# Optimization experiments

Hardware: AMD Instinct MI355X
Metric: run time of the kernel (lower is better)

The kernel has to match this reference:

```python
import jax, jax.numpy as jnp
import numpy as np

NQ = 4      # n_qubits
NL = 1      # n_layers
IN_DIM = 512
HIDDEN = 256
B = 131072


def _apply_1q(state, gate, q, batched):
    """Apply a single-qubit gate on qubit q. state: [B, 2**NQ] complex.
    gate: [2,2] (shared) or [B,2,2] (per-sample)."""
    Bsz = state.shape[0]
    left, right = 2 ** q, 2 ** (NQ - q - 1)
    s = state.reshape(Bsz, left, 2, right)
    if batched:
        s = jnp.einsum('bij,bljr->blir', gate, s)
    else:
        s = jnp.einsum('ij,bljr->blir', gate, s)
    return s.reshape(Bsz, -1)


def _cnot_adjacent(state, q):
    """CNOT with control q, target q+1 (adjacent wires only)."""
    Bsz = state.shape[0]
    left, right = 2 ** q, 2 ** (NQ - q - 2)
    s = state.reshape(Bsz, left, 2, 2, right)
    # control=0 branch unchanged; control=1 branch has target flipped
    s = jnp.stack([s[:, :, 0], s[:, :, 1, ::-1]], axis=2)
    return s.reshape(Bsz, -1)


def _rot_gate(phi, theta, omega):
    """PennyLane Rot(phi,theta,omega) = RZ(omega) RY(theta) RZ(phi)."""
    c, s = jnp.cos(theta / 2), jnp.sin(theta / 2)
    ep = jnp.exp(-0.5j * (phi + omega).astype(jnp.complex64))
    em = jnp.exp(-0.5j * (phi - omega).astype(jnp.complex64))
    return jnp.array([[1.0, 0.0], [0.0, 0.0]], jnp.complex64) * (ep * c) + \
           jnp.array([[0.0, -1.0], [0.0, 0.0]], jnp.complex64) * (jnp.conj(em) * s) + \
           jnp.array([[0.0, 0.0], [1.0, 0.0]], jnp.complex64) * (em * s) + \
           jnp.array([[0.0, 0.0], [0.0, 1.0]], jnp.complex64) * (jnp.conj(ep) * c)


def quantum_circuit(angles, weights):
    """Batched statevector simulation. angles: [B, NQ] float, weights: [NL, NQ, 3].
    Returns PauliZ expectations per qubit: [B, NQ] float32."""
    Bsz = angles.shape[0]
    state = jnp.zeros((Bsz, 2 ** NQ), jnp.complex64).at[:, 0].set(1.0)
    # Angle embedding: RY(inputs[i]) on wire i
    for q in range(NQ):
        th = angles[:, q] / 2
        c, sn = jnp.cos(th), jnp.sin(th)
        g = jnp.stack([jnp.stack([c, -sn], -1), jnp.stack([sn, c], -1)], -2).astype(jnp.complex64)  # [B,2,2]
        state = _apply_1q(state, g, q, batched=True)
    # Entangling layers
    for l in range(NL):
        for q in range(NQ):
            g = _rot_gate(weights[l, q, 0], weights[l, q, 1], weights[l, q, 2])
            state = _apply_1q(state, g, q, batched=False)
        for q in range(NQ - 1):
            state = _cnot_adjacent(state, q)
    # <Z_q> = p(q=0) - p(q=1)
    probs = (jnp.abs(state) ** 2).reshape((Bsz,) + (2,) * NQ)
    outs = []
    for q in range(NQ):
        pq = jnp.moveaxis(probs, 1 + q, -1).reshape(Bsz, -1, 2).sum(1)
        outs.append(pq[:, 0] - pq[:, 1])
    return jnp.stack(outs, -1).astype(jnp.float32)


def setup_inputs() -> dict:
    key = jax.random.key(0)
    ks = jax.random.split(key, 10)
    sc1 = 1.0 / np.sqrt(IN_DIM)
    sch = 1.0 / np.sqrt(HIDDEN)
    scq = 1.0 / np.sqrt(NQ)
    return {
        'x': jax.random.normal(ks[0], (B, IN_DIM), jnp.float32),
        'W1': jax.random.uniform(ks[1], (IN_DIM, HIDDEN), jnp.float32, -sc1, sc1),
        'b1': jax.random.uniform(ks[2], (HIDDEN,), jnp.float32, -sc1, sc1),
        'qparams': jax.random.normal(ks[3], (NL, NQ, 3), jnp.float32),
        'Wr': jax.random.uniform(ks[4], (NQ, HIDDEN), jnp.float32, -scq, scq),
        'br': jax.random.uniform(ks[5], (HIDDEN,), jnp.float32, -scq, scq),
        'W2': jax.random.uniform(ks[6], (HIDDEN, HIDDEN), jnp.float32, -sch, sch),
        'b2': jax.random.uniform(ks[7], (HIDDEN,), jnp.float32, -sch, sch),
        'W3': jax.random.uniform(ks[8], (HIDDEN, HIDDEN), jnp.float32, -sch, sch),
        'b3': jax.random.uniform(ks[9], (HIDDEN,), jnp.float32, -sch, sch),
    }


def reference(x, W1, b1, qparams, Wr, br, W2, b2, W3, b3):
    # Linear -> ReLU -> (Dropout: identity in eval)
    h = jax.nn.relu(x @ W1 + b1)                       # [B, HIDDEN]
    # QuantumLinear: circuit uses first NQ features as RY angles, then readout
    q = quantum_circuit(h[:, :NQ], qparams)            # [B, NQ]
    h = jax.nn.relu(q @ Wr + br)                       # [B, HIDDEN]
    # depth-2 = 1 extra hidden block
    h = jax.nn.relu(h @ W2 + b2)
    return h @ W3 + b3                                 # [B, HIDDEN]
```

## Files before the change

kernel.cpp:

```cpp
#include <hip/hip_runtime.h>

typedef float  f32x4  __attribute__((ext_vector_type(4)));
typedef short  short8 __attribute__((ext_vector_type(8)));

#define BM   32
#define LPAD 264

__device__ __forceinline__ unsigned short f2bf(float f){
  union { float f; unsigned int u; } v; v.f = f;
  unsigned int u = v.u;
  return (unsigned short)((u + 0x7FFFu + ((u >> 16) & 1u)) >> 16);
}
__device__ __forceinline__ float bf2f(unsigned short h){
  union { unsigned int u; float f; } v; v.u = ((unsigned int)h) << 16;
  return v.f;
}

__global__ __launch_bounds__(256) void prep_kernel(
    const float* __restrict__ W1, const float* __restrict__ W2,
    const float* __restrict__ W3, float* __restrict__ w1c,
    unsigned short* __restrict__ W2H, unsigned short* __restrict__ W3H)
{
  int t = blockIdx.x * 256 + threadIdx.x;
  if (t < 2048) {
    w1c[t] = W1[(t >> 2) * 256 + (t & 3)];
  } else if (t < 2048 + 65536) {
    int f = t - 2048;
    int j = f & 7, lane = (f >> 3) & 63, ks = (f >> 9) & 7, n16 = f >> 12;
    int k = ks * 32 + (lane >> 4) * 8 + j;
    int n = n16 * 16 + (lane & 15);
    W2H[f] = f2bf(W2[k * 256 + n]);
  } else if (t < 2048 + 2 * 65536) {
    int f = t - 2048 - 65536;
    int j = f & 7, lane = (f >> 3) & 63, ks = (f >> 9) & 7, n16 = f >> 12;
    int k = ks * 32 + (lane >> 4) * 8 + j;
    int n = n16 * 16 + (lane & 15);
    W3H[f] = f2bf(W3[k * 256 + n]);
  }
}

__global__ __launch_bounds__(256) void angle_kernel(
    const float* __restrict__ x, const float* __restrict__ b1,
    const float* __restrict__ qp, const float* __restrict__ w1c,
    float* __restrict__ z)
{
  const int row = blockIdx.x * 256 + threadIdx.x;
  const f32x4* xr = (const f32x4*)(x + (size_t)row * 512);
  const f32x4* w1 = (const f32x4*)w1c;
  f32x4 p = {0.f, 0.f, 0.f, 0.f};
  #pragma unroll 8
  for (int i = 0; i < 128; i++) {
    f32x4 xa = xr[i];
    p += xa[0] * w1[4 * i + 0];
    p += xa[1] * w1[4 * i + 1];
    p += xa[2] * w1[4 * i + 2];
    p += xa[3] * w1[4 * i + 3];
  }
  float a0 = fmaxf(p[0] + b1[0], 0.f);
  float a1 = fmaxf(p[1] + b1[1], 0.f);
  float a2 = fmaxf(p[2] + b1[2], 0.f);
  float a3 = fmaxf(p[3] + b1[3], 0.f);

  float g00r[4], g00i[4], g01r[4], g01i[4], g10r[4], g10i[4], g11r[4], g11i[4];
  #pragma unroll
  for (int q = 0; q < 4; q++) {
    float phi = qp[q * 3 + 0], th = qp[q * 3 + 1], om = qp[q * 3 + 2];
    float c = cosf(0.5f * th), s = sinf(0.5f * th);
    float A1 = 0.5f * (phi + om), A2 = 0.5f * (phi - om);
    float c1 = cosf(A1), s1 = sinf(A1), c2 = cosf(A2), s2 = sinf(A2);
    g00r[q] =  c * c1;  g00i[q] = -c * s1;
    g01r[q] = -s * c2;  g01i[q] = -s * s2;
    g10r[q] =  s * c2;  g10i[q] = -s * s2;
    g11r[q] =  c * c1;  g11i[q] =  c * s1;
  }
  float cr0 = cosf(0.5f * a0), sv0 = sinf(0.5f * a0);
  float cr1 = cosf(0.5f * a1), sv1 = sinf(0.5f * a1);
  float cr2 = cosf(0.5f * a2), sv2 = sinf(0.5f * a2);
  float cr3 = cosf(0.5f * a3), sv3 = sinf(0.5f * a3);
  float sr[16], si[16];
  #pragma unroll
  for (int i = 0; i < 16; i++) {
    float v = ((i & 8) ? sv0 : cr0) * ((i & 4) ? sv1 : cr1) *
              ((i & 2) ? sv2 : cr2) * ((i & 1) ? sv3 : cr3);
    sr[i] = v; si[i] = 0.f;
  }
  #pragma unroll
  for (int q = 0; q < 4; q++) {
    const int st = 8 >> q;
    #pragma unroll
    for (int i = 0; i < 16; i++) {
      if (i & st) continue;
      const int i1 = i + st;
      float xr_ = sr[i], xi_ = si[i], yr_ = sr[i1], yi_ = si[i1];
      sr[i]  = g00r[q] * xr_ - g00i[q] * xi_ + g01r[q] * yr_ - g01i[q] * yi_;
      si[i]  = g00r[q] * xi_ + g00i[q] * xr_ + g01r[q] * yi_ + g01i[q] * yr_;
      sr[i1] = g10r[q] * xr_ - g10i[q] * xi_ + g11r[q] * yr_ - g11i[q] * yi_;
      si[i1] = g10r[q] * xi_ + g10i[q] * xr_ + g11r[q] * yi_ + g11i[q] * yr_;
    }
  }
  #pragma unroll
  for (int q = 0; q < 3; q++) {
    const int cb = 8 >> q, tb = 4 >> q;
    #pragma unroll
    for (int i = 0; i < 16; i++) {
      if ((i & cb) && !(i & tb)) {
        const int j = i | tb;
        float t1 = sr[i]; sr[i] = sr[j]; sr[j] = t1;
        float t2 = si[i]; si[i] = si[j]; si[j] = t2;
      }
    }
  }
  float z0 = 0.f, z1 = 0.f, z2 = 0.f, z3 = 0.f;
  #pragma unroll
  for (int i = 0; i < 16; i++) {
    float pb = sr[i] * sr[i] + si[i] * si[i];
    z0 += (i & 8) ? -pb : pb;
    z1 += (i & 4) ? -pb : pb;
    z2 += (i & 2) ? -pb : pb;
    z3 += (i & 1) ? -pb : pb;
  }
  f32x4 zv = {z0, z1, z2, z3};
  ((f32x4*)z)[row] = zv;
}

__global__ __launch_bounds__(256, 4) void mlp_kernel(
    const float* __restrict__ z,  const float* __restrict__ Wr,
    const float* __restrict__ br, const float* __restrict__ b2,
    const float* __restrict__ b3,
    const unsigned short* __restrict__ W2H,
    const unsigned short* __restrict__ W3H,
    float* __restrict__ out)
{
  __shared__ __align__(16) char smem[512 + 2 * BM * LPAD * 2];
  f32x4* zl = (f32x4*)smem;
  unsigned short* a_hi = (unsigned short*)(smem + 512);
  unsigned short* a_lo = (unsigned short*)(smem + 512 + BM * LPAD * 2);
  float* fstage = (float*)(smem + 512);

  const int tid = threadIdx.x;
  const int w = tid >> 6, lane = tid & 63;
  const int l15 = lane & 15, l4 = lane >> 4;
  const int row0 = blockIdx.x * BM;

  if (tid < BM) zl[tid] = ((const f32x4*)z)[row0 + tid];
  __syncthreads();

  {
    float wr0 = Wr[tid], wr1 = Wr[256 + tid], wr2 = Wr[512 + tid], wr3 = Wr[768 + tid];
    float brv = br[tid];
    #pragma unroll 4
    for (int rr = 0; rr < BM; rr++) {
      f32x4 zz = zl[rr];
      float hv = fmaf(zz[0], wr0, fmaf(zz[1], wr1, fmaf(zz[2], wr2, fmaf(zz[3], wr3, brv))));
      hv = fmaxf(hv, 0.f);
      unsigned short hi = f2bf(hv);
      a_hi[rr * LPAD + tid] = hi;
      a_lo[rr * LPAD + tid] = f2bf(hv - bf2f(hi));
    }
  }
  __syncthreads();

  f32x4 acc[2][4];
  #pragma unroll
  for (int m = 0; m < 2; m++)
    #pragma unroll
    for (int n = 0; n < 4; n++) acc[m][n] = 0.f;
  #pragma unroll
  for (int ks = 0; ks < 8; ks++) {
    short8 ah[2], al[2];
    #pragma unroll
    for (int m = 0; m < 2; m++) {
      ah[m] = *(const short8*)&a_hi[(m * 16 + l15) * LPAD + ks * 32 + l4 * 8];
      al[m] = *(const short8*)&a_lo[(m * 16 + l15) * LPAD + ks * 32 + l4 * 8];
    }
    #pragma unroll
    for (int nf = 0; nf < 4; nf++) {
      short8 bh = *(const short8*)&W2H[(size_t)(((w * 4 + nf) * 8 + ks) * 64 + lane) * 8];
      #pragma unroll
      for (int m = 0; m < 2; m++) {
        acc[m][nf] = __builtin_amdgcn_mfma_f32_16x16x32_bf16(ah[m], bh, acc[m][nf], 0, 0, 0);
        acc[m][nf] = __builtin_amdgcn_mfma_f32_16x16x32_bf16(al[m], bh, acc[m][nf], 0, 0, 0);
      }
    }
  }
  __syncthreads();

  #pragma unroll
  for (int nf = 0; nf < 4; nf++) {
    int col = w * 64 + nf * 16 + l15;
    float b2v = b2[col];
    #pragma unroll
    for (int m = 0; m < 2; m++)
      #pragma unroll
      for (int i = 0; i < 4; i++) {
        float hv = fmaxf(acc[m][nf][i] + b2v, 0.f);
        unsigned short hi = f2bf(hv);
        int idx = (m * 16 + l4 * 4 + i) * LPAD + col;
        a_hi[idx] = hi;
        a_lo[idx] = f2bf(hv - bf2f(hi));
      }
  }
  __syncthreads();

  #pragma unroll
  for (int m = 0; m < 2; m++)
    #pragma unroll
    for (int n = 0; n < 4; n++) acc[m][n] = 0.f;
  #pragma unroll
  for (int ks = 0; ks < 8; ks++) {
    short8 ah[2], al[2];
    #pragma unroll
    for (int m = 0; m < 2; m++) {
      ah[m] = *(const short8*)&a_hi[(m * 16 + l15) * LPAD + ks * 32 + l4 * 8];
      al[m] = *(const short8*)&a_lo[(m * 16 + l15) * LPAD + ks * 32 + l4 * 8];
    }
    #pragma unroll
    for (int nf = 0; nf < 4; nf++) {
      short8 bh = *(const short8*)&W3H[(size_t)(((w * 4 + nf) * 8 + ks) * 64 + lane) * 8];
      #pragma unroll
      for (int m = 0; m < 2; m++) {
        acc[m][nf] = __builtin_amdgcn_mfma_f32_16x16x32_bf16(ah[m], bh, acc[m][nf], 0, 0, 0);
        acc[m][nf] = __builtin_amdgcn_mfma_f32_16x16x32_bf16(al[m], bh, acc[m][nf], 0, 0, 0);
      }
    }
  }
  __syncthreads();

  #pragma unroll
  for (int nf = 0; nf < 4; nf++) {
    int col = w * 64 + nf * 16 + l15;
    float b3v = b3[col];
    #pragma unroll
    for (int m = 0; m < 2; m++)
      #pragma unroll
      for (int i = 0; i < 4; i++)
        fstage[(m * 16 + l4 * 4 + i) * 260 + col] = acc[m][nf][i] + b3v;
  }
  __syncthreads();
  #pragma unroll
  for (int rr = 0; rr < 8; rr++) {
    int row = w * 8 + rr;
    f32x4 v = ((const f32x4*)&fstage[row * 260])[lane];
    ((f32x4*)(out + (size_t)(row0 + row) * 256))[lane] = v;
  }
}

extern "C" void kernel_launch(void* const* d_in, const int* in_sizes, int n_in,
                              void* d_out, int out_size, void* d_ws, size_t ws_size,
                              hipStream_t stream)
{
  const float* x  = (const float*)d_in[0];
  const float* W1 = (const float*)d_in[1];
  const float* b1 = (const float*)d_in[2];
  const float* qp = (const float*)d_in[3];
  const float* Wr = (const float*)d_in[4];
  const float* br = (const float*)d_in[5];
  const float* W2 = (const float*)d_in[6];
  const float* b2 = (const float*)d_in[7];
  const float* W3 = (const float*)d_in[8];
  const float* b3 = (const float*)d_in[9];
  float* out = (float*)d_out;

  char* ws = (char*)d_ws;
  float* w1c          = (float*)ws;
  unsigned short* W2H = (unsigned short*)(ws + 8192);
  unsigned short* W3H = (unsigned short*)(ws + 8192 + 1 * 131072);
  float* z            = (float*)(ws + 8192 + 2 * 131072);

  prep_kernel<<<520, 256, 0, stream>>>(W1, W2, W3, w1c, W2H, W3H);
  angle_kernel<<<512, 256, 0, stream>>>(x, b1, qp, w1c, z);
  mlp_kernel<<<4096, 256, 0, stream>>>(z, Wr, br, b2, b3, W2H, W3H, out);
}
```

Measured before the change: 175.6 us.

## Fuse angle/quantum kernel with MLP kernel into one persistent-per-256-rows kernel

Merges the per-row angle and statevector computation with the MFMA MLP into a single kernel. Each block handles 256 rows, computing the quantum expectations into shared memory and then looping over 8 tiles of 32 rows for the readout and the two bf16 split-precision GEMMs. This removes the intermediate z buffer in global memory and one kernel launch. In exchange, the grid shrinks from 4096 to 512 blocks and each block processes its tiles serially, which reduces parallelism and latency hiding.

```diff
diff --git a/kernel.cpp b/kernel.cpp
--- a/kernel.cpp
+++ b/kernel.cpp
@@ -39,209 +39,206 @@
   }
 }
 
-__global__ __launch_bounds__(256) void angle_kernel(
-    const float* __restrict__ x, const float* __restrict__ b1,
+__global__ __launch_bounds__(256) void fused_kernel(
+    const float* __restrict__ x,  const float* __restrict__ b1,
     const float* __restrict__ qp, const float* __restrict__ w1c,
-    float* __restrict__ z)
-{
-  const int row = blockIdx.x * 256 + threadIdx.x;
-  const f32x4* xr = (const f32x4*)(x + (size_t)row * 512);
-  const f32x4* w1 = (const f32x4*)w1c;
-  f32x4 p = {0.f, 0.f, 0.f, 0.f};
-  #pragma unroll 8
-  for (int i = 0; i < 128; i++) {
-    f32x4 xa = xr[i];
-    p += xa[0] * w1[4 * i + 0];
-    p += xa[1] * w1[4 * i + 1];
-    p += xa[2] * w1[4 * i + 2];
-    p += xa[3] * w1[4 * i + 3];
-  }
-  float a0 = fmaxf(p[0] + b1[0], 0.f);
-  float a1 = fmaxf(p[1] + b1[1], 0.f);
-  float a2 = fmaxf(p[2] + b1[2], 0.f);
-  float a3 = fmaxf(p[3] + b1[3], 0.f);
-
-  float g00r[4], g00i[4], g01r[4], g01i[4], g10r[4], g10i[4], g11r[4], g11i[4];
-  #pragma unroll
-  for (int q = 0; q < 4; q++) {
-    float phi = qp[q * 3 + 0], th = qp[q * 3 + 1], om = qp[q * 3 + 2];
-    float c = cosf(0.5f * th), s = sinf(0.5f * th);
-    float A1 = 0.5f * (phi + om), A2 = 0.5f * (phi - om);
-    float c1 = cosf(A1), s1 = sinf(A1), c2 = cosf(A2), s2 = sinf(A2);
-    g00r[q] =  c * c1;  g00i[q] = -c * s1;
-    g01r[q] = -s * c2;  g01i[q] = -s * s2;
-    g10r[q] =  s * c2;  g10i[q] = -s * s2;
-    g11r[q] =  c * c1;  g11i[q] =  c * s1;
-  }
-  float cr0 = cosf(0.5f * a0), sv0 = sinf(0.5f * a0);
-  float cr1 = cosf(0.5f * a1), sv1 = sinf(0.5f * a1);
-  float cr2 = cosf(0.5f * a2), sv2 = sinf(0.5f * a2);
-  float cr3 = cosf(0.5f * a3), sv3 = sinf(0.5f * a3);
-  float sr[16], si[16];
-  #pragma unroll
-  for (int i = 0; i < 16; i++) {
-    float v = ((i & 8) ? sv0 : cr0) * ((i & 4) ? sv1 : cr1) *
-              ((i & 2) ? sv2 : cr2) * ((i & 1) ? sv3 : cr3);
-    sr[i] = v; si[i] = 0.f;
-  }
-  #pragma unroll
-  for (int q = 0; q < 4; q++) {
-    const int st = 8 >> q;
-    #pragma unroll
-    for (int i = 0; i < 16; i++) {
-      if (i & st) continue;
-      const int i1 = i + st;
-      float xr_ = sr[i], xi_ = si[i], yr_ = sr[i1], yi_ = si[i1];
-      sr[i]  = g00r[q] * xr_ - g00i[q] * xi_ + g01r[q] * yr_ - g01i[q] * yi_;
-      si[i]  = g00r[q] * xi_ + g00i[q] * xr_ + g01r[q] * yi_ + g01i[q] * yr_;
-      sr[i1] = g10r[q] * xr_ - g10i[q] * xi_ + g11r[q] * yr_ - g11i[q] * yi_;
-      si[i1] = g10r[q] * xi_ + g10i[q] * xr_ + g11r[q] * yi_ + g11i[q] * yr_;
-    }
-  }
-  #pragma unroll
-  for (int q = 0; q < 3; q++) {
-    const int cb = 8 >> q, tb = 4 >> q;
-    #pragma unroll
-    for (int i = 0; i < 16; i++) {
-      if ((i & cb) && !(i & tb)) {
-        const int j = i | tb;
-        float t1 = sr[i]; sr[i] = sr[j]; sr[j] = t1;
-        float t2 = si[i]; si[i] = si[j]; si[j] = t2;
-      }
-    }
-  }
-  float z0 = 0.f, z1 = 0.f, z2 = 0.f, z3 = 0.f;
-  #pragma unroll
-  for (int i = 0; i < 16; i++) {
-    float pb = sr[i] * sr[i] + si[i] * si[i];
-    z0 += (i & 8) ? -pb : pb;
-    z1 += (i & 4) ? -pb : pb;
-    z2 += (i & 2) ? -pb : pb;
-    z3 += (i & 1) ? -pb : pb;
-  }
-  f32x4 zv = {z0, z1, z2, z3};
-  ((f32x4*)z)[row] = zv;
-}
-
-__global__ __launch_bounds__(256, 4) void mlp_kernel(
-    const float* __restrict__ z,  const float* __restrict__ Wr,
-    const float* __restrict__ br, const float* __restrict__ b2,
-    const float* __restrict__ b3,
+    const float* __restrict__ Wr, const float* __restrict__ br,
+    const float* __restrict__ b2, const float* __restrict__ b3,
     const unsigned short* __restrict__ W2H,
     const unsigned short* __restrict__ W3H,
     float* __restrict__ out)
 {
-  __shared__ __align__(16) char smem[512 + 2 * BM * LPAD * 2];
+  __shared__ __align__(16) char smem[4096 + 2 * BM * LPAD * 2];
   f32x4* zl = (f32x4*)smem;
-  unsigned short* a_hi = (unsigned short*)(smem + 512);
-  unsigned short* a_lo = (unsigned short*)(smem + 512 + BM * LPAD * 2);
-  float* fstage = (float*)(smem + 512);
+  unsigned short* a_hi = (unsigned short*)(smem + 4096);
+  unsigned short* a_lo = (unsigned short*)(smem + 4096 + BM * LPAD * 2);
+  float* fstage = (float*)(smem + 4096);
 
   const int tid = threadIdx.x;
   const int w = tid >> 6, lane = tid & 63;
   const int l15 = lane & 15, l4 = lane >> 4;
-  const int row0 = blockIdx.x * BM;
-
-  if (tid < BM) zl[tid] = ((const f32x4*)z)[row0 + tid];
+  const int row0 = blockIdx.x * 256;
+
+  {
+    const int row = row0 + tid;
+    const f32x4* xr = (const f32x4*)(x + (size_t)row * 512);
+    const f32x4* w1 = (const f32x4*)w1c;
+    f32x4 p = {0.f, 0.f, 0.f, 0.f};
+    #pragma unroll 8
+    for (int i = 0; i < 128; i++) {
+      f32x4 xa = xr[i];
+      p += xa[0] * w1[4 * i + 0];
+      p += xa[1] * w1[4 * i + 1];
+      p += xa[2] * w1[4 * i + 2];
+      p += xa[3] * w1[4 * i + 3];
+    }
+    float a0 = fmaxf(p[0] + b1[0], 0.f);
+    float a1 = fmaxf(p[1] + b1[1], 0.f);
+    float a2 = fmaxf(p[2] + b1[2], 0.f);
+    float a3 = fmaxf(p[3] + b1[3], 0.f);
+
+    float g00r[4], g00i[4], g01r[4], g01i[4], g10r[4], g10i[4], g11r[4], g11i[4];
+    #pragma unroll
+    for (int q = 0; q < 4; q++) {
+      float phi = qp[q * 3 + 0], th = qp[q * 3 + 1], om = qp[q * 3 + 2];
+      float c = cosf(0.5f * th), s = sinf(0.5f * th);
+      float A1 = 0.5f * (phi + om), A2 = 0.5f * (phi - om);
+      float c1 = cosf(A1), s1 = sinf(A1), c2 = cosf(A2), s2 = sinf(A2);
+      g00r[q] =  c * c1;  g00i[q] = -c * s1;
+      g01r[q] = -s * c2;  g01i[q] = -s * s2;
+      g10r[q] =  s * c2;  g10i[q] = -s * s2;
+      g11r[q] =  c * c1;  g11i[q] =  c * s1;
+    }
+    float cr0 = cosf(0.5f * a0), sv0 = sinf(0.5f * a0);
+    float cr1 = cosf(0.5f * a1), sv1 = sinf(0.5f * a1);
+    float cr2 = cosf(0.5f * a2), sv2 = sinf(0.5f * a2);
+    float cr3 = cosf(0.5f * a3), sv3 = sinf(0.5f * a3);
+    float sr[16], si[16];
+    #pragma unroll
+    for (int i = 0; i < 16; i++) {
+      float v = ((i & 8) ? sv0 : cr0) * ((i & 4) ? sv1 : cr1) *
+                ((i & 2) ? sv2 : cr2) * ((i & 1) ? sv3 : cr3);
+      sr[i] = v; si[i] = 0.f;
+    }
+    #pragma unroll
+    for (int q = 0; q < 4; q++) {
+      const int st = 8 >> q;
+      #pragma unroll
+      for (int i = 0; i < 16; i++) {
+        if (i & st) continue;
+        const int i1 = i + st;
+        float xr_ = sr[i], xi_ = si[i], yr_ = sr[i1], yi_ = si[i1];
+        sr[i]  = g00r[q] * xr_ - g00i[q] * xi_ + g01r[q] * yr_ - g01i[q] * yi_;
+        si[i]  = g00r[q] * xi_ + g00i[q] * xr_ + g01r[q] * yi_ + g01i[q] * yr_;
+        sr[i1] = g10r[q] * xr_ - g10i[q] * xi_ + g11r[q] * yr_ - g11i[q] * yi_;
+        si[i1] = g10r[q] * xi_ + g10i[q] * xr_ + g11r[q] * yi_ + g11i[q] * yr_;
+      }
+    }
+    #pragma unroll
+    for (int q = 0; q < 3; q++) {
+      const int cb = 8 >> q, tb = 4 >> q;
+      #pragma unroll
+      for (int i = 0; i < 16; i++) {
+        if ((i & cb) && !(i & tb)) {
+          const int j = i | tb;
+          float t1 = sr[i]; sr[i] = sr[j]; sr[j] = t1;
+          float t2 = si[i]; si[i] = si[j]; si[j] = t2;
+        }
+      }
+    }
+    float z0 = 0.f, z1 = 0.f, z2 = 0.f, z3 = 0.f;
+    #pragma unroll
+    for (int i = 0; i < 16; i++) {
+      float pb = sr[i] * sr[i] + si[i] * si[i];
+      z0 += (i & 8) ? -pb : pb;
+      z1 += (i & 4) ? -pb : pb;
+      z2 += (i & 2) ? -pb : pb;
+      z3 += (i & 1) ? -pb : pb;
+    }
+    f32x4 zv = {z0, z1, z2, z3};
+    zl[tid] = zv;
+  }
   __syncthreads();
 
-  {
-    float wr0 = Wr[tid], wr1 = Wr[256 + tid], wr2 = Wr[512 + tid], wr3 = Wr[768 + tid];
-    float brv = br[tid];
+  const float wr0 = Wr[tid], wr1 = Wr[256 + tid], wr2 = Wr[512 + tid], wr3 = Wr[768 + tid];
+  const float brv = br[tid];
+
+  for (int mt = 0; mt < 8; mt++) {
     #pragma unroll 4
     for (int rr = 0; rr < BM; rr++) {
-      f32x4 zz = zl[rr];
+      f32x4 zz = zl[mt * 32 + rr];
       float hv = fmaf(zz[0], wr0, fmaf(zz[1], wr1, fmaf(zz[2], wr2, fmaf(zz[3], wr3, brv))));
       hv = fmaxf(hv, 0.f);
       unsigned short hi = f2bf(hv);
       a_hi[rr * LPAD + tid] = hi;
       a_lo[rr * LPAD + tid] = f2bf(hv - bf2f(hi));
     }
-  }
-  __syncthreads();
-
-  f32x4 acc[2][4];
-  #pragma unroll
-  for (int m = 0; m < 2; m++)
-    #pragma unroll
-    for (int n = 0; n < 4; n++) acc[m][n] = 0.f;
-  #pragma unroll
-  for (int ks = 0; ks < 8; ks++) {
-    short8 ah[2], al[2];
-    #pragma unroll
-    for (int m = 0; m < 2; m++) {
-      ah[m] = *(const short8*)&a_hi[(m * 16 + l15) * LPAD + ks * 32 + l4 * 8];
-      al[m] = *(const short8*)&a_lo[(m * 16 + l15) * LPAD + ks * 32 + l4 * 8];
-    }
+    __syncthreads();
+
+    f32x4 acc[2][4];
+    #pragma unroll
+    for (int m = 0; m < 2; m++)
+      #pragma unroll
+      for (int n = 0; n < 4; n++) acc[m][n] = 0.f;
+    #pragma unroll
+    for (int ks = 0; ks < 8; ks++) {
+      short8 ah[2], al[2];
+      #pragma unroll
+      for (int m = 0; m < 2; m++) {
+        ah[m] = *(const short8*)&a_hi[(m * 16 + l15) * LPAD + ks * 32 + l4 * 8];
+        al[m] = *(const short8*)&a_lo[(m * 16 + l15) * LPAD + ks * 32 + l4 * 8];
+      }
+      #pragma unroll
+      for (int nf = 0; nf < 4; nf++) {
+        short8 bh = *(const short8*)&W2H[(size_t)(((w * 4 + nf) * 8 + ks) * 64 + lane) * 8];
+        #pragma unroll
+        for (int m = 0; m < 2; m++) {
+          acc[m][nf] = __builtin_amdgcn_mfma_f32_16x16x32_bf16(ah[m], bh, acc[m][nf], 0, 0, 0);
+          acc[m][nf] = __builtin_amdgcn_mfma_f32_16x16x32_bf16(al[m], bh, acc[m][nf], 0, 0, 0);
+        }
+      }
+    }
+    __syncthreads();
+
     #pragma unroll
     for (int nf = 0; nf < 4; nf++) {
-      short8 bh = *(const short8*)&W2H[(size_t)(((w * 4 + nf) * 8 + ks) * 64 + lane) * 8];
+      int col = w * 64 + nf * 16 + l15;
+      float b2v = b2[col];
+      #pragma unroll
+      for (int m = 0; m < 2; m++)
+        #pragma unroll
+        for (int i = 0; i < 4; i++) {
+          float hv = fmaxf(acc[m][nf][i] + b2v, 0.f);
+          unsigned short hi = f2bf(hv);
+          int idx = (m * 16 + l4 * 4 + i) * LPAD + col;
+          a_hi[idx] = hi;
+          a_lo[idx] = f2bf(hv - bf2f(hi));
+        }
+    }
+    __syncthreads();
+
+    #pragma unroll
+    for (int m = 0; m < 2; m++)
+      #pragma unroll
+      for (int n = 0; n < 4; n++) acc[m][n] = 0.f;
+    #pragma unroll
+    for (int ks = 0; ks < 8; ks++) {
+      short8 ah[2], al[2];
       #pragma unroll
       for (int m = 0; m < 2; m++) {
-        acc[m][nf] = __builtin_amdgcn_mfma_f32_16x16x32_bf16(ah[m], bh, acc[m][nf], 0, 0, 0);
-        acc[m][nf] = __builtin_amdgcn_mfma_f32_16x16x32_bf16(al[m], bh, acc[m][nf], 0, 0, 0);
-      }
-    }
-  }
-  __syncthreads();
-
-  #pragma unroll
-  for (int nf = 0; nf < 4; nf++) {
-    int col = w * 64 + nf * 16 + l15;
-    float b2v = b2[col];
-    #pragma unroll
-    for (int m = 0; m < 2; m++)
-      #pragma unroll
-      for (int i = 0; i < 4; i++) {
-        float hv = fmaxf(acc[m][nf][i] + b2v, 0.f);
-        unsigned short hi = f2bf(hv);
-        int idx = (m * 16 + l4 * 4 + i) * LPAD + col;
-        a_hi[idx] = hi;
-        a_lo[idx] = f2bf(hv - bf2f(hi));
-      }
-  }
-  __syncthreads();
-
-  #pragma unroll
-  for (int m = 0; m < 2; m++)
-    #pragma unroll
-    for (int n = 0; n < 4; n++) acc[m][n] = 0.f;
-  #pragma unroll
-  for (int ks = 0; ks < 8; ks++) {
-    short8 ah[2], al[2];
-    #pragma unroll
-    for (int m = 0; m < 2; m++) {
-      ah[m] = *(const short8*)&a_hi[(m * 16 + l15) * LPAD + ks * 32 + l4 * 8];
-      al[m] = *(const short8*)&a_lo[(m * 16 + l15) * LPAD + ks * 32 + l4 * 8];
-    }
+        ah[m] = *(const short8*)&a_hi[(m * 16 + l15) * LPAD + ks * 32 + l4 * 8];
+        al[m] = *(const short8*)&a_lo[(m * 16 + l15) * LPAD + ks * 32 + l4 * 8];
+      }
+      #pragma unroll
+      for (int nf = 0; nf < 4; nf++) {
+        short8 bh = *(const short8*)&W3H[(size_t)(((w * 4 + nf) * 8 + ks) * 64 + lane) * 8];
+        #pragma unroll
+        for (int m = 0; m < 2; m++) {
+          acc[m][nf] = __builtin_amdgcn_mfma_f32_16x16x32_bf16(ah[m], bh, acc[m][nf], 0, 0, 0);
+          acc[m][nf] = __builtin_amdgcn_mfma_f32_16x16x32_bf16(al[m], bh, acc[m][nf], 0, 0, 0);
+        }
+      }
+    }
+    __syncthreads();
+
     #pragma unroll
     for (int nf = 0; nf < 4; nf++) {
-      short8 bh = *(const short8*)&W3H[(size_t)(((w * 4 + nf) * 8 + ks) * 64 + lane) * 8];
-      #pragma unroll
-      for (int m = 0; m < 2; m++) {
-        acc[m][nf] = __builtin_amdgcn_mfma_f32_16x16x32_bf16(ah[m], bh, acc[m][nf], 0, 0, 0);
-        acc[m][nf] = __builtin_amdgcn_mfma_f32_16x16x32_bf16(al[m], bh, acc[m][nf], 0, 0, 0);
-      }
-    }
-  }
-  __syncthreads();
-
-  #pragma unroll
-  for (int nf = 0; nf < 4; nf++) {
-    int col = w * 64 + nf * 16 + l15;
-    float b3v = b3[col];
-    #pragma unroll
-    for (int m = 0; m < 2; m++)
-      #pragma unroll
-      for (int i = 0; i < 4; i++)
-        fstage[(m * 16 + l4 * 4 + i) * 260 + col] = acc[m][nf][i] + b3v;
-  }
-  __syncthreads();
-  #pragma unroll
-  for (int rr = 0; rr < 8; rr++) {
-    int row = w * 8 + rr;
-    f32x4 v = ((const f32x4*)&fstage[row * 260])[lane];
-    ((f32x4*)(out + (size_t)(row0 + row) * 256))[lane] = v;
+      int col = w * 64 + nf * 16 + l15;
+      float b3v = b3[col];
+      #pragma unroll
+      for (int m = 0; m < 2; m++)
+        #pragma unroll
+        for (int i = 0; i < 4; i++)
+          fstage[(m * 16 + l4 * 4 + i) * 260 + col] = acc[m][nf][i] + b3v;
+    }
+    __syncthreads();
+    #pragma unroll
+    for (int rr = 0; rr < 8; rr++) {
+      int row = w * 8 + rr;
+      f32x4 v = ((const f32x4*)&fstage[row * 260])[lane];
+      ((f32x4*)(out + (size_t)(row0 + mt * 32 + row) * 256))[lane] = v;
+    }
+    __syncthreads();
   }
 }
 
@@ -265,9 +262,8 @@
   float* w1c          = (float*)ws;
   unsigned short* W2H = (unsigned short*)(ws + 8192);
   unsigned short* W3H = (unsigned short*)(ws + 8192 + 1 * 131072);
-  float* z            = (float*)(ws + 8192 + 2 * 131072);
 
   prep_kernel<<<520, 256, 0, stream>>>(W1, W2, W3, w1c, W2H, W3H);
-  angle_kernel<<<512, 256, 0, stream>>>(x, b1, qp, w1c, z);
-  mlp_kernel<<<4096, 256, 0, stream>>>(z, Wr, br, b2, b3, W2H, W3H, out);
-}
+  fused_kernel<<<512, 256, 0, stream>>>(x, b1, qp, w1c, Wr, br, b2, b3,
+                                        W2H, W3H, out);
+}
```

Measured after the change: 202.0 us. 15.0% more time.
